# Performance work log

Hardware: AMD Instinct MI355X
Metric: run time of the kernel (lower is better)

The kernel has to match this reference:

```python
import jax, jax.numpy as jnp
import numpy as np

D_MODEL = 1024
N_HEADS = 16
HEAD_DIM = D_MODEL // N_HEADS
ROPE_BASE = 10000.0


def _rope_cos_sin(t, dtype):
    # inv_freq over half the head dim, standard RoPE (GPT-NeoX style)
    inv_freq = 1.0 / (ROPE_BASE ** (jnp.arange(0, HEAD_DIM, 2, dtype=jnp.float32) / HEAD_DIM))
    freqs = jnp.arange(t, dtype=jnp.float32)[:, None] * inv_freq[None, :]  # [t, hd/2]
    emb = jnp.concatenate([freqs, freqs], axis=-1)  # [t, hd]
    return jnp.cos(emb).astype(dtype), jnp.sin(emb).astype(dtype)


def _rotate_half(x):
    x1, x2 = jnp.split(x, 2, axis=-1)
    return jnp.concatenate([-x2, x1], axis=-1)


def _apply_rope(x, cos, sin):
    # x: [b, h, t, hd]; cos/sin: [t, hd]
    return x * cos[None, None] + _rotate_half(x) * sin[None, None]


def setup_inputs() -> dict:
    key = jax.random.key(0)
    kx, kqkv, kout = jax.random.split(key, 3)
    x = jax.random.normal(kx, (4, 2048, D_MODEL), dtype=jnp.float32)
    scale = 1.0 / np.sqrt(D_MODEL)
    Wqkv = jax.random.normal(kqkv, (D_MODEL, 3 * D_MODEL), dtype=jnp.float32) * scale
    Wout = jax.random.normal(kout, (D_MODEL, D_MODEL), dtype=jnp.float32) * scale
    return {"x": x, "Wqkv": Wqkv, "Wout": Wout}


def reference(x, Wqkv, Wout):
    b, t, _ = x.shape
    qkv = (x @ Wqkv).reshape(b, t, 3, N_HEADS, HEAD_DIM)
    q, k, v = qkv[:, :, 0], qkv[:, :, 1], qkv[:, :, 2]  # [b, t, h, hd]
    q = q.transpose(0, 2, 1, 3)  # [b, h, t, hd]
    k = k.transpose(0, 2, 1, 3)
    v = v.transpose(0, 2, 1, 3)
    cos, sin = _rope_cos_sin(t, x.dtype)
    q = _apply_rope(q, cos, sin)
    k = _apply_rope(k, cos, sin)
    # causal SDPA
    scores = jnp.einsum("bhqd,bhkd->bhqk", q, k) / np.sqrt(HEAD_DIM)
    causal = jnp.tril(jnp.ones((t, t), dtype=bool))
    scores = jnp.where(causal[None, None], scores, jnp.finfo(scores.dtype).min)
    attn = jax.nn.softmax(scores, axis=-1)
    out = jnp.einsum("bhqk,bhkd->bhqd", attn, v)
    out = out.transpose(0, 2, 1, 3).reshape(b, t, D_MODEL)
    return out @ Wout
```

## Files before the change

kernel.cpp:

```cpp
#include <hip/hip_runtime.h>
#include <cstdint>
#include <cstddef>

typedef __bf16 bf16;
typedef __bf16 bf16x8 __attribute__((ext_vector_type(8)));
typedef __bf16 bf16x4 __attribute__((ext_vector_type(4)));
typedef __bf16 bf16x2 __attribute__((ext_vector_type(2)));
typedef float  f32x4  __attribute__((ext_vector_type(4)));
typedef float  f32x16 __attribute__((ext_vector_type(16)));
typedef int    i32x4  __attribute__((ext_vector_type(4)));

#define MFMA16(a, b, c) __builtin_amdgcn_mfma_f32_16x16x32_bf16((a), (b), (c), 0, 0, 0)
#define MFMA32(a, b, c) __builtin_amdgcn_mfma_f32_32x32x16_bf16((a), (b), (c), 0, 0, 0)

static constexpr int BB   = 4;
static constexpr int TT   = 2048;
static constexpr int DM   = 1024;
static constexpr int NH   = 16;
static constexpr int HD   = 64;
static constexpr int TOK  = BB * TT;
static constexpr int NQKV = 3 * DM;

__device__ inline void gload16(const void* g, void* l) {
    __builtin_amdgcn_global_load_lds((const __attribute__((address_space(1))) void*)g,
                                     (__attribute__((address_space(3))) void*)l, 16, 0, 0);
}

__device__ inline int swz(int x) { return x ^ ((x >> 3) & 0x70); }

__device__ inline int pk2(float a, float b) {
    bf16x2 t; t[0] = (bf16)a; t[1] = (bf16)b;
    return __builtin_bit_cast(int, t);
}

__global__ void k_cvt(const float* __restrict__ in, bf16* __restrict__ out, int n) {
    int i = (blockIdx.x * blockDim.x + threadIdx.x) * 4;
    if (i >= n) return;
    float4 v = *(const float4*)(in + i);
    bf16x4 o;
    o[0] = (bf16)v.x; o[1] = (bf16)v.y; o[2] = (bf16)v.z; o[3] = (bf16)v.w;
    *(bf16x4*)(out + i) = o;
}

__global__ void k_transpose_cvt(const float* __restrict__ in, bf16* __restrict__ out,
                                int R, int C) {
    __shared__ bf16 tl[64 * 72];
    int tid = threadIdx.x;
    int c0 = blockIdx.x * 64, r0 = blockIdx.y * 64;
#pragma unroll
    for (int rep = 0; rep < 4; rep++) {
        int r = rep * 16 + (tid >> 4);
        int c = (tid & 15) * 4;
        float4 v = *(const float4*)(in + (size_t)(r0 + r) * C + c0 + c);
        tl[r * 72 + c + 0] = (bf16)v.x;
        tl[r * 72 + c + 1] = (bf16)v.y;
        tl[r * 72 + c + 2] = (bf16)v.z;
        tl[r * 72 + c + 3] = (bf16)v.w;
    }
    __syncthreads();
#pragma unroll
    for (int rep = 0; rep < 4; rep++) {
        int cc = rep * 16 + (tid >> 4);
        int rr = (tid & 15) * 4;
        bf16x4 o;
        o[0] = tl[(rr + 0) * 72 + cc];
        o[1] = tl[(rr + 1) * 72 + cc];
        o[2] = tl[(rr + 2) * 72 + cc];
        o[3] = tl[(rr + 3) * 72 + cc];
        *(bf16x4*)(out + (size_t)(c0 + cc) * R + r0 + rr) = o;
    }
}

__global__ void k_rope_tab(float* __restrict__ ct, float* __restrict__ st) {
    int i = blockIdx.x * blockDim.x + threadIdx.x;
    int t = i >> 5, j = i & 31;
    float invf = powf(10000.0f, -(float)j * (1.0f / 32.0f));
    float a = (float)t * invf;
    ct[i] = cosf(a);
    st[i] = sinf(a);
}

template <int MODE>
__global__ __launch_bounds__(256) void k_gemm_bt(
    const bf16* __restrict__ A, const bf16* __restrict__ Bt,
    int M, int N, int K,
    float* __restrict__ outF,
    bf16* __restrict__ qbuf, bf16* __restrict__ kbuf, bf16* __restrict__ vbuf,
    const float* __restrict__ ct, const float* __restrict__ st, float qscale) {
    __shared__ bf16 lA[2][128 * 64];
    __shared__ bf16 lB[2][128 * 64];
    int tid = threadIdx.x;
    int l = tid & 63, wid = tid >> 6;
    int wm = wid >> 1, wn = wid & 1;
    int bn = blockIdx.x, bm = blockIdx.y;
    const char* AbB = (const char*)(A + (size_t)bm * 128 * K);
    const char* BbB = (const char*)(Bt + (size_t)bn * 128 * K);
    const size_t KB = (size_t)K * 2;
    f32x4 acc[4][4] = {};

#define GSTAGE(nb, kt) do {                                                                \
    _Pragma("unroll") for (int i = 0; i < 4; i++) {                                        \
        int cb = (wid * 4 + i) * 1024;               \
        int Xs = swz(cb + l * 16);                   \
        gload16(AbB + (size_t)(Xs >> 7) * KB + (size_t)(kt) * 2 + (Xs & 127),              \
                (char*)lA[nb] + cb);                                                       \
        gload16(BbB + (size_t)(Xs >> 7) * KB + (size_t)(kt) * 2 + (Xs & 127),              \
                (char*)lB[nb] + cb);                                                       \
    }                                                                                      \
} while (0)

    GSTAGE(0, 0);
    __syncthreads();
    int cur = 0;
    int nsteps = K >> 6;
    for (int t = 0; t < nsteps; t++) {
        if (t + 1 < nsteps) GSTAGE(cur ^ 1, (t + 1) << 6);
#pragma unroll
        for (int kk = 0; kk < 2; kk++) {
            bf16x8 af[4], bfr[4];
#pragma unroll
            for (int mi = 0; mi < 4; mi++) {
                int rr = wm * 64 + mi * 16 + (l & 15);
                int L = rr * 128 + (kk * 32 + (l >> 4) * 8) * 2;
                af[mi] = *(const bf16x8*)((const char*)lA[cur] + swz(L));
            }
#pragma unroll
            for (int ni = 0; ni < 4; ni++) {
                int rr = wn * 64 + ni * 16 + (l & 15);
                int L = rr * 128 + (kk * 32 + (l >> 4) * 8) * 2;
                bfr[ni] = *(const bf16x8*)((const char*)lB[cur] + swz(L));
            }
#pragma unroll
            for (int mi = 0; mi < 4; mi++)
#pragma unroll
                for (int ni = 0; ni < 4; ni++)
                    acc[mi][ni] = MFMA16(af[mi], bfr[ni], acc[mi][ni]);
        }
        __syncthreads();
        cur ^= 1;
    }
#undef GSTAGE

    if (MODE == 2) {
#pragma unroll
        for (int mi = 0; mi < 4; mi++) {
            int m0 = bm * 128 + wm * 64 + mi * 16 + ((l >> 4) << 2);
#pragma unroll
            for (int ni = 0; ni < 4; ni++) {
                int n = bn * 128 + wn * 64 + ni * 16 + (l & 15);
#pragma unroll
                for (int rj = 0; rj < 4; rj++)
                    outF[(size_t)(m0 + rj) * N + n] = acc[mi][ni][rj];
            }
        }
    } else {
        int n0 = bn * 128 + wn * 64;
        int sQ = n0 >> 10;
        int h = (n0 & 1023) >> 6;
        if (sQ == 2) {
#pragma unroll
            for (int ni = 0; ni < 4; ni++) {
                int d = ni * 16 + (l & 15);
#pragma unroll
                for (int mi = 0; mi < 4; mi++) {
                    int m0 = bm * 128 + wm * 64 + mi * 16 + ((l >> 4) << 2);
                    int b = m0 >> 11, t0 = m0 & 2047;
                    bf16x4 pv;
#pragma unroll
                    for (int rj = 0; rj < 4; rj++) pv[rj] = (bf16)acc[mi][ni][rj];
                    *(bf16x4*)(vbuf + ((size_t)((b * NH + h) * HD + d)) * TT + t0) = pv;
                }
            }
        } else {
            float qs = (sQ == 0) ? qscale : 1.0f;
            bf16* obuf = (sQ == 0) ? qbuf : kbuf;
#pragma unroll
            for (int mi = 0; mi < 4; mi++) {
                int m0 = bm * 128 + wm * 64 + mi * 16 + ((l >> 4) << 2);
                int b = m0 >> 11, t0 = m0 & 2047;
#pragma unroll
                for (int rj = 0; rj < 4; rj++) {
                    int t = t0 + rj;
                    bf16* dst = obuf + ((size_t)(b * NH + h) * TT + t) * HD;
                    const float* crow = ct + t * 32;
                    const float* srow = st + t * 32;
#pragma unroll
                    for (int ni2 = 0; ni2 < 2; ni2++) {
                        int d = ni2 * 16 + (l & 15);
                        float cs = crow[d], sn = srow[d];
                        float a  = acc[mi][ni2][rj];
                        float b2 = acc[mi][ni2 + 2][rj];
                        dst[d]      = (bf16)(qs * (a  * cs - b2 * sn));
                        dst[d + 32] = (bf16)(qs * (b2 * cs + a  * sn));
                    }
                }
            }
        }
    }
}

__global__ __launch_bounds__(256, 2) void k_attn(
    const bf16* __restrict__ Q, const bf16* __restrict__ K,
    const bf16* __restrict__ Vt, bf16* __restrict__ O) {
    __shared__ bf16 lK[2][4096];
    __shared__ bf16 lV[2][4096];
    int tid = threadIdx.x;
    int l = tid & 63, w = tid >> 6;
    int bx = blockIdx.x, by = blockIdx.y;
    int bh = bx * 8 + (by >> 4);
    int s = 15 - (by & 15);
    const char* KbB = (const char*)(K + (size_t)bh * TT * HD);
    const char* VbB = (const char*)(Vt + (size_t)bh * HD * TT);
    int b = bh >> 4, h = bh & 15;

    bf16x8 ones;
#pragma unroll
    for (int e = 0; e < 8; e++) ones[e] = (bf16)1.0f;

#define STAGE_KV(nb, j) do {                                                               \
    int X0_ = w * 1024 + l * 16;                                                           \
    const char* Kj_ = KbB + (size_t)(j) * 8192;                                            \
    gload16(Kj_ + swz(X0_),        (char*)lK[nb] + w * 1024);                              \
    gload16(Kj_ + swz(X0_ + 4096), (char*)lK[nb] + w * 1024 + 4096);                       \
    int o0_ = swz(X0_), o1_ = swz(X0_ + 4096);                                             \
    gload16(VbB + (size_t)(o0_ >> 7) * (TT * 2) + (size_t)(j) * 128 + (o0_ & 127),         \
            (char*)lV[nb] + w * 1024);                                                     \
    gload16(VbB + (size_t)(o1_ >> 7) * (TT * 2) + (size_t)(j) * 128 + (o1_ & 127),         \
            (char*)lV[nb] + w * 1024 + 4096);                                              \
} while (0)

    int r0 = s * 128;
    int nblk = 2 * s + 2;
    int wrow = r0 + w * 32;
    const bf16* Qb = Q + ((size_t)bh * TT + wrow) * HD;
    bf16x8 qa[4];
#pragma unroll
    for (int kc = 0; kc < 4; kc++)
        qa[kc] = *(const bf16x8*)(Qb + (size_t)(l & 31) * HD + kc * 16 + (l >> 5) * 8);

    f32x16 oacc[2] = {};
    f32x16 lacc = {};

    STAGE_KV(0, 0);
    __syncthreads();
    int cur = 0;
    for (int j = 0; j < nblk; j++) {
        if (j + 1 < nblk) STAGE_KV(cur ^ 1, j + 1);
        if (j * 64 <= wrow + 31) {
            f32x16 sc[2];
#pragma unroll
            for (int r = 0; r < 16; r++) { sc[0][r] = -16.0f; sc[1][r] = -16.0f; }
            __builtin_amdgcn_s_setprio(1);
#pragma unroll
            for (int kc = 0; kc < 4; kc++)
#pragma unroll
                for (int nj = 0; nj < 2; nj++) {
                    int rr = nj * 32 + (l & 31);
                    int L = rr * 128 + ((kc * 16 + (l >> 5) * 8) * 2 ^ ((rr & 7) << 4));
                    bf16x8 kb = *(const bf16x8*)((const char*)lK[cur] + L);
                    sc[nj] = MFMA32(kb, qa[kc], sc[nj]);
                }
            __builtin_amdgcn_s_setprio(0);
            if (j * 64 + 63 > wrow) {
                int q = wrow + (l & 31);
#pragma unroll
                for (int nj = 0; nj < 2; nj++)
#pragma unroll
                    for (int r = 0; r < 16; r++) {
                        int kvg = j * 64 + nj * 32 + (r & 3) + 8 * (r >> 2) + 4 * (l >> 5);
                        if (kvg > q) sc[nj][r] = -1e30f;
                    }
            }
#pragma unroll
            for (int nj = 0; nj < 2; nj++)
#pragma unroll
                for (int r = 0; r < 16; r++)
                    sc[nj][r] = exp2f(sc[nj][r]);
            __builtin_amdgcn_s_setprio(1);
#pragma unroll
            for (int c = 0; c < 4; c++) {
                const int nj = c >> 1, rb = (c & 1) * 8;
                int w0 = pk2(sc[nj][rb + 0], sc[nj][rb + 1]);
                int w1 = pk2(sc[nj][rb + 2], sc[nj][rb + 3]);
                int w2 = pk2(sc[nj][rb + 4], sc[nj][rb + 5]);
                int w3 = pk2(sc[nj][rb + 6], sc[nj][rb + 7]);
                asm("v_permlane32_swap_b32 %0, %1" : "+v"(w0), "+v"(w2));
                asm("v_permlane32_swap_b32 %0, %1" : "+v"(w1), "+v"(w3));
                i32x4 fw; fw[0] = w0; fw[1] = w1; fw[2] = w2; fw[3] = w3;
                bf16x8 pa = __builtin_bit_cast(bf16x8, fw);
                lacc = MFMA32(pa, ones, lacc);
#pragma unroll
                for (int dt = 0; dt < 2; dt++) {
                    int dd = dt * 32 + (l & 31);
                    int L = dd * 128 + ((c * 16 + (l >> 5) * 8) * 2 ^ ((dd & 7) << 4));
                    bf16x8 vbf = *(const bf16x8*)((const char*)lV[cur] + L);
                    oacc[dt] = MFMA32(pa, vbf, oacc[dt]);
                }
            }
            __builtin_amdgcn_s_setprio(0);
        }
        __syncthreads();
        cur ^= 1;
    }
#pragma unroll
    for (int r = 0; r < 16; r++) {
        int rq = (r & 3) + 8 * (r >> 2) + 4 * (l >> 5);
        int t = wrow + rq;
        float inv = 1.0f / lacc[r];
        size_t base = ((size_t)b * TT + t) * DM + h * HD;
#pragma unroll
        for (int dt = 0; dt < 2; dt++)
            O[base + dt * 32 + (l & 31)] = (bf16)(oacc[dt][r] * inv);
    }
#undef STAGE_KV
}

extern "C" void kernel_launch(void* const* d_in, const int* in_sizes, int n_in,
                              void* d_out, int out_size, void* d_ws, size_t ws_size,
                              hipStream_t stream) {
    const float* x    = (const float*)d_in[0];
    const float* Wqkv = (const float*)d_in[1];
    const float* Wout = (const float*)d_in[2];
    float* out = (float*)d_out;

    char* ws = (char*)d_ws;
    size_t off = 0;
    auto alloc = [&](size_t bytes) {
        void* p = ws + off;
        off += (bytes + 255) & ~(size_t)255;
        return p;
    };
    bf16* xb    = (bf16*)alloc((size_t)TOK * DM * 2);
    bf16* wqkvt = (bf16*)alloc((size_t)NQKV * DM * 2);
    bf16* woutt = (bf16*)alloc((size_t)DM * DM * 2);
    bf16* qr    = (bf16*)alloc((size_t)TOK * DM * 2);
    bf16* kr    = (bf16*)alloc((size_t)TOK * DM * 2);
    bf16* vt    = (bf16*)alloc((size_t)TOK * DM * 2);
    bf16* ob    = (bf16*)alloc((size_t)TOK * DM * 2);
    float* ct   = (float*)alloc((size_t)TT * 32 * 4);
    float* st   = (float*)alloc((size_t)TT * 32 * 4);
    (void)ws_size; (void)in_sizes; (void)n_in; (void)out_size;

    k_cvt<<<TOK * DM / 4 / 256, 256, 0, stream>>>(x, xb, TOK * DM);
    k_transpose_cvt<<<dim3(NQKV / 64, DM / 64), 256, 0, stream>>>(Wqkv, wqkvt, DM, NQKV);
    k_transpose_cvt<<<dim3(DM / 64, DM / 64), 256, 0, stream>>>(Wout, woutt, DM, DM);
    k_rope_tab<<<TT * 32 / 256, 256, 0, stream>>>(ct, st);
    k_gemm_bt<1><<<dim3(NQKV / 128, TOK / 128), 256, 0, stream>>>(
        xb, wqkvt, TOK, NQKV, DM, nullptr, qr, kr, vt,
        ct, st, 0.125f * 1.4426950408889634f);
    k_attn<<<dim3(8, 128), 256, 0, stream>>>(qr, kr, vt, ob);
    k_gemm_bt<2><<<dim3(DM / 128, TOK / 128), 256, 0, stream>>>(
        ob, woutt, TOK, DM, DM, out, nullptr, nullptr, nullptr,
        nullptr, nullptr, 0.0f);
}
```

Before: 200.3 us.

## Pair causal query tiles per block and route P through LDS

Each attention block now handles two query tiles (s and 15-s) in sequence, so every block does the same causal workload and the grid is halved. The P matrix is no longer rearranged in registers with permlane swaps; it is written to a swizzled LDS buffer and read back as the MFMA A operand. The pairing targets tail imbalance from causal blocks of uneven length. The LDS round trip adds shared-memory traffic and 16KB more LDS per block, which may lower occupancy. There is also no barrier between the lP writes and reads, which relies on each wave touching only its own rows.

```diff
diff --git a/kernel.cpp b/kernel.cpp
--- a/kernel.cpp
+++ b/kernel.cpp
@@ -8,7 +8,6 @@
 typedef __bf16 bf16x2 __attribute__((ext_vector_type(2)));
 typedef float  f32x4  __attribute__((ext_vector_type(4)));
 typedef float  f32x16 __attribute__((ext_vector_type(16)));
-typedef int    i32x4  __attribute__((ext_vector_type(4)));
 
 #define MFMA16(a, b, c) __builtin_amdgcn_mfma_f32_16x16x32_bf16((a), (b), (c), 0, 0, 0)
 #define MFMA32(a, b, c) __builtin_amdgcn_mfma_f32_32x32x16_bf16((a), (b), (c), 0, 0, 0)
@@ -204,11 +203,12 @@
     const bf16* __restrict__ Vt, bf16* __restrict__ O) {
     __shared__ bf16 lK[2][4096];
     __shared__ bf16 lV[2][4096];
+    __shared__ bf16 lP[8192];
     int tid = threadIdx.x;
     int l = tid & 63, w = tid >> 6;
     int bx = blockIdx.x, by = blockIdx.y;
-    int bh = bx * 8 + (by >> 4);
-    int s = 15 - (by & 15);
+    int bh = bx * 8 + (by >> 3);
+    int p = by & 7;
     const char* KbB = (const char*)(K + (size_t)bh * TT * HD);
     const char* VbB = (const char*)(Vt + (size_t)bh * HD * TT);
     int b = bh >> 4, h = bh & 15;
@@ -216,6 +216,11 @@
     bf16x8 ones;
 #pragma unroll
     for (int e = 0; e < 8; e++) ones[e] = (bf16)1.0f;
+
+    int prow = w * 32 + (l & 31);
+    int pwbase = prow * 128;
+    int pswzk = (prow & 7) << 4;
+    int cbase = (l >> 5) * 8;
 
 #define STAGE_KV(nb, j) do {                                                               \
     int X0_ = w * 1024 + l * 16;                                                           \
@@ -229,88 +234,94 @@
             (char*)lV[nb] + w * 1024 + 4096);                                              \
 } while (0)
 
-    int r0 = s * 128;
-    int nblk = 2 * s + 2;
-    int wrow = r0 + w * 32;
-    const bf16* Qb = Q + ((size_t)bh * TT + wrow) * HD;
-    bf16x8 qa[4];
-#pragma unroll
-    for (int kc = 0; kc < 4; kc++)
-        qa[kc] = *(const bf16x8*)(Qb + (size_t)(l & 31) * HD + kc * 16 + (l >> 5) * 8);
-
-    f32x16 oacc[2] = {};
-    f32x16 lacc = {};
-
-    STAGE_KV(0, 0);
-    __syncthreads();
-    int cur = 0;
-    for (int j = 0; j < nblk; j++) {
-        if (j + 1 < nblk) STAGE_KV(cur ^ 1, j + 1);
-        if (j * 64 <= wrow + 31) {
-            f32x16 sc[2];
-#pragma unroll
-            for (int r = 0; r < 16; r++) { sc[0][r] = -16.0f; sc[1][r] = -16.0f; }
-            __builtin_amdgcn_s_setprio(1);
-#pragma unroll
-            for (int kc = 0; kc < 4; kc++)
-#pragma unroll
-                for (int nj = 0; nj < 2; nj++) {
-                    int rr = nj * 32 + (l & 31);
-                    int L = rr * 128 + ((kc * 16 + (l >> 5) * 8) * 2 ^ ((rr & 7) << 4));
-                    bf16x8 kb = *(const bf16x8*)((const char*)lK[cur] + L);
-                    sc[nj] = MFMA32(kb, qa[kc], sc[nj]);
+    for (int half = 0; half < 2; half++) {
+        int s = (half == 0) ? (15 - p) : p;
+        int r0 = s * 128;
+        int nblk = 2 * s + 2;
+        int wrow = r0 + w * 32;
+        const bf16* Qb = Q + ((size_t)bh * TT + wrow) * HD;
+        bf16x8 qa[4];
+#pragma unroll
+        for (int kc = 0; kc < 4; kc++)
+            qa[kc] = *(const bf16x8*)(Qb + (size_t)(l & 31) * HD + kc * 16 + (l >> 5) * 8);
+
+        f32x16 oacc[2] = {};
+        f32x16 lacc = {};
+
+        STAGE_KV(0, 0);
+        __syncthreads();
+        int cur = 0;
+        for (int j = 0; j < nblk; j++) {
+            if (j + 1 < nblk) STAGE_KV(cur ^ 1, j + 1);
+            if (j * 64 <= wrow + 31) {
+                f32x16 sc[2];
+#pragma unroll
+                for (int r = 0; r < 16; r++) { sc[0][r] = -16.0f; sc[1][r] = -16.0f; }
+                __builtin_amdgcn_s_setprio(1);
+#pragma unroll
+                for (int kc = 0; kc < 4; kc++)
+#pragma unroll
+                    for (int nj = 0; nj < 2; nj++) {
+                        int rr = nj * 32 + (l & 31);
+                        int L = rr * 128 + ((kc * 16 + (l >> 5) * 8) * 2 ^ ((rr & 7) << 4));
+                        bf16x8 kb = *(const bf16x8*)((const char*)lK[cur] + L);
+                        sc[nj] = MFMA32(kb, qa[kc], sc[nj]);
+                    }
+                __builtin_amdgcn_s_setprio(0);
+                if (j * 64 + 63 > wrow) {
+                    int q = wrow + (l & 31);
+#pragma unroll
+                    for (int nj = 0; nj < 2; nj++)
+#pragma unroll
+                        for (int r = 0; r < 16; r++) {
+                            int kvg = j * 64 + nj * 32 + (r & 3) + 8 * (r >> 2) + 4 * (l >> 5);
+                            if (kvg > q) sc[nj][r] = -1e30f;
+                        }
                 }
-            __builtin_amdgcn_s_setprio(0);
-            if (j * 64 + 63 > wrow) {
-                int q = wrow + (l & 31);
 #pragma unroll
                 for (int nj = 0; nj < 2; nj++)
 #pragma unroll
-                    for (int r = 0; r < 16; r++) {
-                        int kvg = j * 64 + nj * 32 + (r & 3) + 8 * (r >> 2) + 4 * (l >> 5);
-                        if (kvg > q) sc[nj][r] = -1e30f;
+                    for (int r = 0; r < 16; r++)
+                        sc[nj][r] = exp2f(sc[nj][r]);
+#pragma unroll
+                for (int nj = 0; nj < 2; nj++)
+#pragma unroll
+                    for (int qd = 0; qd < 4; qd++) {
+                        int2 v2;
+                        v2.x = pk2(sc[nj][qd * 4 + 0], sc[nj][qd * 4 + 1]);
+                        v2.y = pk2(sc[nj][qd * 4 + 2], sc[nj][qd * 4 + 3]);
+                        int col2 = nj * 64 + qd * 16 + cbase;
+                        *(int2*)((char*)lP + pwbase + (col2 ^ pswzk)) = v2;
                     }
-            }
-#pragma unroll
-            for (int nj = 0; nj < 2; nj++)
-#pragma unroll
-                for (int r = 0; r < 16; r++)
-                    sc[nj][r] = exp2f(sc[nj][r]);
-            __builtin_amdgcn_s_setprio(1);
-#pragma unroll
-            for (int c = 0; c < 4; c++) {
-                const int nj = c >> 1, rb = (c & 1) * 8;
-                int w0 = pk2(sc[nj][rb + 0], sc[nj][rb + 1]);
-                int w1 = pk2(sc[nj][rb + 2], sc[nj][rb + 3]);
-                int w2 = pk2(sc[nj][rb + 4], sc[nj][rb + 5]);
-                int w3 = pk2(sc[nj][rb + 6], sc[nj][rb + 7]);
-                asm("v_permlane32_swap_b32 %0, %1" : "+v"(w0), "+v"(w2));
-                asm("v_permlane32_swap_b32 %0, %1" : "+v"(w1), "+v"(w3));
-                i32x4 fw; fw[0] = w0; fw[1] = w1; fw[2] = w2; fw[3] = w3;
-                bf16x8 pa = __builtin_bit_cast(bf16x8, fw);
-                lacc = MFMA32(pa, ones, lacc);
-#pragma unroll
-                for (int dt = 0; dt < 2; dt++) {
-                    int dd = dt * 32 + (l & 31);
-                    int L = dd * 128 + ((c * 16 + (l >> 5) * 8) * 2 ^ ((dd & 7) << 4));
-                    bf16x8 vbf = *(const bf16x8*)((const char*)lV[cur] + L);
-                    oacc[dt] = MFMA32(pa, vbf, oacc[dt]);
+                __builtin_amdgcn_s_setprio(1);
+#pragma unroll
+                for (int kc = 0; kc < 4; kc++) {
+                    bf16x8 pa = *(const bf16x8*)((const char*)lP + pwbase
+                                 + ((kc * 32 + (l >> 5) * 16) ^ pswzk));
+                    lacc = MFMA32(pa, ones, lacc);
+#pragma unroll
+                    for (int dt = 0; dt < 2; dt++) {
+                        int dd = dt * 32 + (l & 31);
+                        int L = dd * 128 + ((kc * 16 + (l >> 5) * 8) * 2 ^ ((dd & 7) << 4));
+                        bf16x8 vbf = *(const bf16x8*)((const char*)lV[cur] + L);
+                        oacc[dt] = MFMA32(pa, vbf, oacc[dt]);
+                    }
                 }
-            }
-            __builtin_amdgcn_s_setprio(0);
-        }
-        __syncthreads();
-        cur ^= 1;
-    }
-#pragma unroll
-    for (int r = 0; r < 16; r++) {
-        int rq = (r & 3) + 8 * (r >> 2) + 4 * (l >> 5);
-        int t = wrow + rq;
-        float inv = 1.0f / lacc[r];
-        size_t base = ((size_t)b * TT + t) * DM + h * HD;
-#pragma unroll
-        for (int dt = 0; dt < 2; dt++)
-            O[base + dt * 32 + (l & 31)] = (bf16)(oacc[dt][r] * inv);
+                __builtin_amdgcn_s_setprio(0);
+            }
+            __syncthreads();
+            cur ^= 1;
+        }
+#pragma unroll
+        for (int r = 0; r < 16; r++) {
+            int rq = (r & 3) + 8 * (r >> 2) + 4 * (l >> 5);
+            int t = wrow + rq;
+            float inv = 1.0f / lacc[r];
+            size_t base = ((size_t)b * TT + t) * DM + h * HD;
+#pragma unroll
+            for (int dt = 0; dt < 2; dt++)
+                O[base + dt * 32 + (l & 31)] = (bf16)(oacc[dt][r] * inv);
+        }
     }
 #undef STAGE_KV
 }
@@ -348,7 +359,7 @@
     k_gemm_bt<1><<<dim3(NQKV / 128, TOK / 128), 256, 0, stream>>>(
         xb, wqkvt, TOK, NQKV, DM, nullptr, qr, kr, vt,
         ct, st, 0.125f * 1.4426950408889634f);
-    k_attn<<<dim3(8, 128), 256, 0, stream>>>(qr, kr, vt, ob);
+    k_attn<<<dim3(8, 64), 256, 0, stream>>>(qr, kr, vt, ob);
     k_gemm_bt<2><<<dim3(DM / 128, TOK / 128), 256, 0, stream>>>(
         ob, woutt, TOK, DM, DM, out, nullptr, nullptr, nullptr,
         nullptr, nullptr, 0.0f);
```

Result: faster. 185.7 us (-7.3%).
